# Performance work log

Measured on AMD Instinct MI355X. Metric: run time of the kernel, lower is better.

## Reference

```python
import jax, jax.numpy as jnp
import numpy as np

S = 4096      # seq_len
D = 1024      # d_model
H = 16        # n_heads
E = 64        # head dim (D // H)
SCALE0 = 1.0 / np.sqrt(E)  # sh_scale_factor


def setup_inputs() -> dict:
    key = jax.random.key(0)
    ks = jax.random.split(key, 10)
    std = 1.0 / np.sqrt(D)
    inputs = jax.random.normal(ks[0], (S, D), dtype=jnp.float32)
    # per-head projection weights stacked over heads: [H, D, E]
    Wq = jax.random.normal(ks[1], (H, D, E), dtype=jnp.float32) * std
    bq = jnp.zeros((H, E), dtype=jnp.float32)
    Wk = jax.random.normal(ks[2], (H, D, E), dtype=jnp.float32) * std
    bk = jnp.zeros((H, E), dtype=jnp.float32)
    Wv = jax.random.normal(ks[3], (H, D, E), dtype=jnp.float32) * std
    bv = jnp.zeros((H, E), dtype=jnp.float32)
    # learned per-head scalar scale, initialized to 1/sqrt(E)
    scale = jnp.full((H,), SCALE0, dtype=jnp.float32)
    # output projection (stored as [D_in, D_out])
    Wo = jax.random.normal(ks[4], (H * E, D), dtype=jnp.float32) * std
    bo = jnp.zeros((D,), dtype=jnp.float32)
    return {"inputs": inputs, "Wq": Wq, "bq": bq, "Wk": Wk, "bk": bk,
            "Wv": Wv, "bv": bv, "scale": scale, "Wo": Wo, "bo": bo}


def reference(inputs, Wq, bq, Wk, bk, Wv, bv, scale, Wo, bo):
    # per-head QKV projections, batched over heads: [H, S, E]
    q = jnp.einsum('sd,hde->hse', inputs, Wq) + bq[:, None, :]
    k = jnp.einsum('sd,hde->hse', inputs, Wk) + bk[:, None, :]
    v = jnp.einsum('sd,hde->hse', inputs, Wv) + bv[:, None, :]
    # scores [H, S, S], learned scalar scale per head, softmax over keys
    scores = jnp.einsum('hqe,hke->hqk', q, k) * scale[:, None, None]
    attn = jax.nn.softmax(scores, axis=-1)
    o = jnp.einsum('hqk,hke->hqe', attn, v)           # [H, S, E]
    o = jnp.transpose(o, (1, 0, 2)).reshape(S, H * E)  # concat heads on dim 1
    return o @ Wo + bo                                 # [S, D]
```

## Files before the change

kernel.cpp:

```cpp
#include <hip/hip_runtime.h>
#include <stdint.h>

#define S_LEN 4096
#define D_MOD 1024
#define NH    16
#define EH    64

typedef short bf16x8 __attribute__((ext_vector_type(8)));
typedef float f32x4  __attribute__((ext_vector_type(4)));
typedef float f32x16 __attribute__((ext_vector_type(16)));

__device__ __forceinline__ unsigned short f2b(float x){
    uint32_t u = __float_as_uint(x);
    u = (u + 0x7fffu + ((u >> 16) & 1u)) >> 16;
    return (unsigned short)u;
}

__device__ __forceinline__ uint32_t cvtpk_bf16(float lo, float hi){
    uint32_t r;
    asm volatile("v_cvt_pk_bf16_f32 %0, %1, %2" : "=v"(r) : "v"(lo), "v"(hi));
    return r;
}

__device__ __forceinline__ void gld_lds16(const void* g, void* l){
    __builtin_amdgcn_global_load_lds((const __attribute__((address_space(1))) void*)g,
                                     (__attribute__((address_space(3))) void*)l, 16, 0, 0);
}

#define PSWAP_U(a, b) asm volatile("v_permlane32_swap_b32 %0, %1" : "+v"(a), "+v"(b))

__device__ __forceinline__ float vcopy(float x){
    float y;
    asm volatile("v_mov_b32 %0, %1" : "=v"(y) : "v"(x));
    return y;
}
__device__ __forceinline__ float pswap_add(float x){
    uint32_t a = __float_as_uint(x), b = __float_as_uint(vcopy(x));
    PSWAP_U(a, b);
    return __uint_as_float(a) + __uint_as_float(b);
}

#define WAITV4() asm volatile("s_waitcnt vmcnt(4)" ::: "memory")
#define WAITV0() asm volatile("s_waitcnt vmcnt(0)" ::: "memory")
#define CFENCE() asm volatile("" ::: "memory")


__global__ void k_conv_x(const float* __restrict__ x, unsigned short* __restrict__ xb, int n){
    int i = (blockIdx.x * blockDim.x + threadIdx.x) * 4;
    if (i < n){
        float4 v = *(const float4*)(x + i);
        ushort4 o;
        o.x = f2b(v.x); o.y = f2b(v.y); o.z = f2b(v.z); o.w = f2b(v.w);
        *(ushort4*)(xb + i) = o;
    }
}

__global__ void k_conv_w(const float* __restrict__ Wq, const float* __restrict__ Wk,
                         const float* __restrict__ Wv, unsigned short* __restrict__ wt){
    __shared__ float lt[64][65];
    const int tid = threadIdx.x;
    const int d0 = blockIdx.x * 64;
    const int th = blockIdx.y;
    const int t = th >> 4, h = th & 15;
    const float* W = (t == 0) ? Wq : ((t == 1) ? Wk : Wv);
    #pragma unroll
    for (int i = 0; i < 16; i++){
        int idx = tid + 256 * i;
        int dl = idx >> 6, e = idx & 63;
        lt[dl][e] = W[((size_t)((h << 10) + d0 + dl) << 6) + e];
    }
    __syncthreads();
    #pragma unroll
    for (int i = 0; i < 16; i++){
        int idx = tid + 256 * i;
        int eo = idx >> 6, dlo = idx & 63;
        wt[((size_t)((t << 10) + (h << 6) + eo) << 10) + d0 + dlo] = f2b(lt[dlo][eo]);
    }
}

__global__ void k_conv_wo(const float* __restrict__ Wo, unsigned short* __restrict__ wot){
    __shared__ float lt[64][65];
    const int tid = threadIdx.x;
    const int he0 = blockIdx.x * 64, d0 = blockIdx.y * 64;
    #pragma unroll
    for (int i = 0; i < 16; i++){
        int idx = tid + 256 * i;
        int r = idx >> 6, c = idx & 63;
        lt[r][c] = Wo[((size_t)(he0 + r) << 10) + d0 + c];
    }
    __syncthreads();
    #pragma unroll
    for (int i = 0; i < 16; i++){
        int idx = tid + 256 * i;
        int rr = idx >> 6, cc = idx & 63;
        wot[((size_t)(d0 + rr) << 10) + he0 + cc] = f2b(lt[cc][rr]);
    }
}

__global__ void k_tv(const unsigned short* __restrict__ vr, unsigned short* __restrict__ vt){
    __shared__ unsigned short lt[64][66];
    const int tid = threadIdx.x;
    const int s0 = blockIdx.x * 64, h = blockIdx.y;
    #pragma unroll
    for (int i = 0; i < 4; i++){
        int idx = tid + 256 * i;
        int r = idx >> 4, c4 = idx & 15;
        ushort4 v = *(const ushort4*)(vr + (((size_t)(h << 12) + s0 + r) << 6) + c4 * 4);
        lt[r][c4 * 4 + 0] = v.x; lt[r][c4 * 4 + 1] = v.y;
        lt[r][c4 * 4 + 2] = v.z; lt[r][c4 * 4 + 3] = v.w;
    }
    __syncthreads();
    #pragma unroll
    for (int i = 0; i < 4; i++){
        int idx = tid + 256 * i;
        int e = idx >> 4, j4 = idx & 15;
        ushort4 o;
        o.x = lt[j4 * 4 + 0][e]; o.y = lt[j4 * 4 + 1][e];
        o.z = lt[j4 * 4 + 2][e]; o.w = lt[j4 * 4 + 3][e];
        *(ushort4*)(vt + (size_t)((h << 6) + e) * 4096 + s0 + j4 * 4) = o;
    }
}


template<int MODE, int NI>
__global__ __launch_bounds__(256, 4)
void k_gemm(const unsigned short* __restrict__ A, const unsigned short* __restrict__ B, int K,
            unsigned short* __restrict__ qb, unsigned short* __restrict__ kb,
            unsigned short* __restrict__ vr,
            const float* __restrict__ b0, const float* __restrict__ b1, const float* __restrict__ b2,
            const float* __restrict__ scl,
            float* __restrict__ outp, const float* __restrict__ bo){
    __shared__ uint4 lsA4[1024];
    __shared__ uint4 lsB4[NI * 256];
    char* lsA = (char*)lsA4;
    char* lsB = (char*)lsB4;
    const int tid = threadIdx.x;
    const int lane = tid & 63, w = tid >> 6;
    const int lr = lane & 15, lg = lane >> 4;
    const int wm = w >> 1, wn = w & 1;
    const int m0 = blockIdx.y * 128, n0 = blockIdx.x * (32 * NI);
    const int wbase = tid & ~63;

    f32x4 acc[4][NI] = {};

    for (int k0 = 0; k0 < K; k0 += 64){
        __syncthreads();
        #pragma unroll
        for (int i = 0; i < 4; i++){
            int s = tid + 256 * i;
            int row = s >> 3, c = s & 7;
            int cs = c ^ (row & 7);
            gld_lds16(A + (size_t)(m0 + row) * K + k0 + cs * 8, lsA + (wbase + 256 * i) * 16);
        }
        #pragma unroll
        for (int i = 0; i < NI; i++){
            int s = tid + 256 * i;
            int row = s >> 3, c = s & 7;
            int cs = c ^ (row & 7);
            gld_lds16(B + (size_t)(n0 + row) * K + k0 + cs * 8, lsB + (wbase + 256 * i) * 16);
        }
        __syncthreads();
        #pragma unroll
        for (int kc = 0; kc < 2; kc++){
            bf16x8 af[4], bf[NI];
            #pragma unroll
            for (int mi = 0; mi < 4; mi++){
                int row = wm * 64 + mi * 16 + lr;
                int j = kc * 4 + lg;
                af[mi] = *(const bf16x8*)(lsA + row * 128 + (j ^ (row & 7)) * 16);
            }
            #pragma unroll
            for (int ni = 0; ni < NI; ni++){
                int row = wn * (NI * 16) + ni * 16 + lr;
                int j = kc * 4 + lg;
                bf[ni] = *(const bf16x8*)(lsB + row * 128 + (j ^ (row & 7)) * 16);
            }
            #pragma unroll
            for (int mi = 0; mi < 4; mi++)
                #pragma unroll
                for (int ni = 0; ni < NI; ni++)
                    acc[mi][ni] = __builtin_amdgcn_mfma_f32_16x16x32_bf16(af[mi], bf[ni], acc[mi][ni], 0, 0, 0);
        }
    }

    #pragma unroll
    for (int mi = 0; mi < 4; mi++){
        #pragma unroll
        for (int ni = 0; ni < NI; ni++){
            int gnb = n0 + wn * (NI * 16) + ni * 16;
            if (MODE == 0){
                int t = gnb >> 10, h = (gnb >> 6) & 15;
                int e = (gnb & 63) + lr;
                const float* bp = (t == 0) ? b0 : ((t == 1) ? b1 : b2);
                float badd = bp[(h << 6) + e];
                float qs = (t == 0) ? scl[h] * 1.4426950408889634f : 1.0f;
                unsigned short* tgt = (t == 0) ? qb : ((t == 1) ? kb : vr);
                #pragma unroll
                for (int r = 0; r < 4; r++){
                    int gm = m0 + wm * 64 + mi * 16 + lg * 4 + r;
                    tgt[((size_t)((h << 12) + gm) << 6) + e] = f2b((acc[mi][ni][r] + badd) * qs);
                }
            } else {
                int gn = gnb + lr;
                float badd = bo[gn];
                #pragma unroll
                for (int r = 0; r < 4; r++){
                    int gm = m0 + wm * 64 + mi * 16 + lg * 4 + r;
                    outp[(size_t)gm * 1024 + gn] = acc[mi][ni][r] + badd;
                }
            }
        }
    }
}


__global__ __launch_bounds__(256, 4)
void k_attn(const unsigned short* __restrict__ qb, const unsigned short* __restrict__ kb,
            const unsigned short* __restrict__ vt,
            unsigned short* __restrict__ po0, unsigned short* __restrict__ po1,
            float* __restrict__ pl){
    __shared__ uint4 ldsb[2048];
    char* ldsc = (char*)ldsb;

    const int tid = threadIdx.x;
    const int lane = tid & 63, w = tid >> 6;
    const int ql = lane & 31, hi = lane >> 5;

    int wg = blockIdx.y * 64 + blockIdx.x;
    wg = (wg & 7) * 128 + (wg >> 3);
    const int h = wg >> 6;
    const int qblk = (wg & 63) >> 1;
    const int sk = wg & 1;
    const int q0 = qblk * 128 + w * 32;
    const int kbase = sk * 2048;

    bf16x8 qf[4];
    #pragma unroll
    for (int kc = 0; kc < 4; kc++)
        qf[kc] = *(const bf16x8*)(qb + (size_t)((h << 12) + q0 + ql) * 64 + kc * 16 + hi * 8);

    f32x16 oacc[2] = {};
    float l_run = 0.f;

    auto stage = [&](int buf, int kt){
        char* Kd = ldsc + buf * 16384;
        char* Vd = Kd + 8192;
        #pragma unroll
        for (int c = 0; c < 2; c++){
            int g = w * 2 + c;
            const unsigned short* ksrc = kb + ((size_t)(h << 12) + kt + (g >> 2) * 32 + ql) * 64
                                            + (g & 3) * 16 + hi * 8;
            gld_lds16(ksrc, Kd + g * 1024);
            const unsigned short* vsrc = vt + (size_t)((h << 6) + (g >> 2) * 32 + ql) * 4096
                                            + kt + (g & 3) * 16 + hi * 8;
            gld_lds16(vsrc, Vd + g * 1024);
        }
    };

    stage(0, kbase);
    stage(1, kbase + 64);

    int buf = 0;
    for (int t = 0; t < 32; t++){
        if (t < 31) WAITV4();
        else        WAITV0();
        __builtin_amdgcn_s_barrier();
        CFENCE();

        const char* Kc = ldsc + buf * 16384;
        const char* Vc = Kc + 8192;

        f32x16 s[2];
        __builtin_amdgcn_s_setprio(1);
        #pragma unroll
        for (int kt2 = 0; kt2 < 2; kt2++){
            f32x16 sx = {};
            #pragma unroll
            for (int kc = 0; kc < 4; kc++){
                bf16x8 kf = *(const bf16x8*)(Kc + (kt2 * 4 + kc) * 1024 + lane * 16);
                sx = __builtin_amdgcn_mfma_f32_32x32x16_bf16(kf, qf[kc], sx, 0, 0, 0);
            }
            s[kt2] = sx;
        }
        __builtin_amdgcn_s_setprio(0);

        #pragma unroll
        for (int kt2 = 0; kt2 < 2; kt2++){
            f32x16& v = s[kt2];
            #pragma unroll
            for (int r = 0; r < 16; r++){
                v[r] = __builtin_amdgcn_exp2f(v[r]);
                l_run += v[r];
            }
            uint32_t a0 = cvtpk_bf16(v[0], v[1]);
            uint32_t a1 = cvtpk_bf16(v[2], v[3]);
            uint32_t b0 = cvtpk_bf16(v[4], v[5]);
            uint32_t b1 = cvtpk_bf16(v[6], v[7]);
            PSWAP_U(a0, b0);
            PSWAP_U(a1, b1);
            uint32_t f0[4] = {a0, a1, b0, b1};
            bf16x8 p0 = *(bf16x8*)f0;
            uint32_t c0 = cvtpk_bf16(v[8],  v[9]);
            uint32_t c1 = cvtpk_bf16(v[10], v[11]);
            uint32_t d0 = cvtpk_bf16(v[12], v[13]);
            uint32_t d1 = cvtpk_bf16(v[14], v[15]);
            PSWAP_U(c0, d0);
            PSWAP_U(c1, d1);
            uint32_t f1[4] = {c0, c1, d0, d1};
            bf16x8 p1 = *(bf16x8*)f1;

            #pragma unroll
            for (int et = 0; et < 2; et++){
                bf16x8 vf0 = *(const bf16x8*)(Vc + (et * 4 + kt2 * 2) * 1024 + lane * 16);
                oacc[et] = __builtin_amdgcn_mfma_f32_32x32x16_bf16(vf0, p0, oacc[et], 0, 0, 0);
                bf16x8 vf1 = *(const bf16x8*)(Vc + (et * 4 + kt2 * 2 + 1) * 1024 + lane * 16);
                oacc[et] = __builtin_amdgcn_mfma_f32_32x32x16_bf16(vf1, p1, oacc[et], 0, 0, 0);
            }
        }
        CFENCE();

        if (t + 2 < 32){
            __builtin_amdgcn_s_barrier();
            CFENCE();
            stage(buf, kbase + (t + 2) * 64);
        }
        buf ^= 1;
    }

    unsigned short* pout = sk ? po1 : po0;
    float l = pswap_add(l_run);
    if (lane < 32)
        pl[((sk << 4) + h) * 4096 + q0 + ql] = l;
    #pragma unroll
    for (int et = 0; et < 2; et++){
        #pragma unroll
        for (int g = 0; g < 4; g++){
            ushort4 o4;
            o4.x = f2b(oacc[et][4 * g + 0]);
            o4.y = f2b(oacc[et][4 * g + 1]);
            o4.z = f2b(oacc[et][4 * g + 2]);
            o4.w = f2b(oacc[et][4 * g + 3]);
            int e = et * 32 + 8 * g + 4 * hi;
            *(ushort4*)(pout + (size_t)(q0 + ql) * 1024 + (h << 6) + e) = o4;
        }
    }
}

__global__ void k_comb(const unsigned short* __restrict__ po0, const unsigned short* __restrict__ po1,
                       const float* __restrict__ pl, unsigned short* __restrict__ ob){
    int i = blockIdx.x * 256 + threadIdx.x;
    int s = i >> 7, g8 = i & 127;
    int h = g8 >> 3;
    float inv = 1.0f / (pl[(h << 12) + s] + pl[((16 + h) << 12) + s]);
    size_t off = ((size_t)s << 10) + g8 * 8;
    const ushort4* a = (const ushort4*)(po0 + off);
    const ushort4* b = (const ushort4*)(po1 + off);
    ushort4 o[2];
    #pragma unroll
    for (int k = 0; k < 2; k++){
        ushort4 av = a[k], bv = b[k];
        o[k].x = f2b((__uint_as_float((uint32_t)av.x << 16) + __uint_as_float((uint32_t)bv.x << 16)) * inv);
        o[k].y = f2b((__uint_as_float((uint32_t)av.y << 16) + __uint_as_float((uint32_t)bv.y << 16)) * inv);
        o[k].z = f2b((__uint_as_float((uint32_t)av.z << 16) + __uint_as_float((uint32_t)bv.z << 16)) * inv);
        o[k].w = f2b((__uint_as_float((uint32_t)av.w << 16) + __uint_as_float((uint32_t)bv.w << 16)) * inv);
    }
    *(ushort4*)(ob + off) = o[0];
    *(ushort4*)(ob + off + 4) = o[1];
}


extern "C" void kernel_launch(void* const* d_in, const int* in_sizes, int n_in,
                              void* d_out, int out_size, void* d_ws, size_t ws_size,
                              hipStream_t stream){
    const float* x  = (const float*)d_in[0];
    const float* Wq = (const float*)d_in[1];
    const float* bq = (const float*)d_in[2];
    const float* Wk = (const float*)d_in[3];
    const float* bk = (const float*)d_in[4];
    const float* Wv = (const float*)d_in[5];
    const float* bv = (const float*)d_in[6];
    const float* sc = (const float*)d_in[7];
    const float* Wo = (const float*)d_in[8];
    const float* bo = (const float*)d_in[9];
    float* out = (float*)d_out;
    char* ws = (char*)d_ws;
    const size_t MB = 1u << 20;

    unsigned short* xb  = (unsigned short*)(ws + 0);
    unsigned short* ob  = xb;
    unsigned short* wt  = (unsigned short*)(ws + 8  * MB);
    unsigned short* wot = (unsigned short*)(ws + 14 * MB);
    unsigned short* qb  = (unsigned short*)(ws + 16 * MB);
    unsigned short* kb  = (unsigned short*)(ws + 24 * MB);
    unsigned short* vr  = (unsigned short*)(ws + 32 * MB);
    unsigned short* po0 = vr;
    unsigned short* vt  = (unsigned short*)(ws + 40 * MB);
    unsigned short* po1 = (unsigned short*)(ws + 48 * MB);
    float*          pl  = (float*)(ws + 56 * MB);

    k_conv_x <<<4096, 256, 0, stream>>>(x, xb, S_LEN * D_MOD);
    k_conv_w <<<dim3(16, 48), 256, 0, stream>>>(Wq, Wk, Wv, wt);
    k_conv_wo<<<dim3(16, 16), 256, 0, stream>>>(Wo, wot);

    k_gemm<0, 4><<<dim3(24, 32), 256, 0, stream>>>(xb, wt, D_MOD, qb, kb, vr, bq, bk, bv, sc, nullptr, nullptr);
    k_tv        <<<dim3(64, 16), 256, 0, stream>>>(vr, vt);
    k_attn      <<<dim3(64, 16), 256, 0, stream>>>(qb, kb, vt, po0, po1, pl);
    k_comb      <<<2048, 256, 0, stream>>>(po0, po1, pl, ob);
    k_gemm<1, 2><<<dim3(16, 32), 256, 0, stream>>>(ob, wot, D_MOD, nullptr, nullptr, nullptr,
                                                   nullptr, nullptr, nullptr, nullptr, out, bo);
}
```

Baseline: 162.8 us.

## Merge conversion kernels and compute softmax row sums via ones-MFMA

Three conversion kernels (x, QKV weights, Wo) become one launch that picks its role from the block index, removing two launch gaps. In attention, the running softmax denominator is no longer a per-element VALU sum plus a final cross-lane reduce. It is accumulated by extra MFMAs against a vector of bf16 ones, which offloads VALU work to the matrix unit. The QK and PV stages are also interleaved per 32-key half so the exp/pack of one half can overlap matrix work. This adds 4 MFMAs per tile and sums bf16-rounded probabilities instead of fp32 values, a small accuracy change.

```diff
diff --git a/kernel.cpp b/kernel.cpp
--- a/kernel.cpp
+++ b/kernel.cpp
@@ -29,71 +29,61 @@
 
 #define PSWAP_U(a, b) asm volatile("v_permlane32_swap_b32 %0, %1" : "+v"(a), "+v"(b))
 
-__device__ __forceinline__ float vcopy(float x){
-    float y;
-    asm volatile("v_mov_b32 %0, %1" : "=v"(y) : "v"(x));
-    return y;
-}
-__device__ __forceinline__ float pswap_add(float x){
-    uint32_t a = __float_as_uint(x), b = __float_as_uint(vcopy(x));
-    PSWAP_U(a, b);
-    return __uint_as_float(a) + __uint_as_float(b);
-}
-
 #define WAITV4() asm volatile("s_waitcnt vmcnt(4)" ::: "memory")
 #define WAITV0() asm volatile("s_waitcnt vmcnt(0)" ::: "memory")
 #define CFENCE() asm volatile("" ::: "memory")
 
 
-__global__ void k_conv_x(const float* __restrict__ x, unsigned short* __restrict__ xb, int n){
-    int i = (blockIdx.x * blockDim.x + threadIdx.x) * 4;
-    if (i < n){
+__global__ void k_conv_all(const float* __restrict__ x, unsigned short* __restrict__ xb,
+                           const float* __restrict__ Wq, const float* __restrict__ Wk,
+                           const float* __restrict__ Wv, unsigned short* __restrict__ wt,
+                           const float* __restrict__ Wo, unsigned short* __restrict__ wot){
+    __shared__ float lt[64][65];
+    const int tid = threadIdx.x;
+    int b = blockIdx.x;
+    if (b < 4096){
+        int i = (b * 256 + tid) * 4;
         float4 v = *(const float4*)(x + i);
         ushort4 o;
         o.x = f2b(v.x); o.y = f2b(v.y); o.z = f2b(v.z); o.w = f2b(v.w);
         *(ushort4*)(xb + i) = o;
-    }
-}
-
-__global__ void k_conv_w(const float* __restrict__ Wq, const float* __restrict__ Wk,
-                         const float* __restrict__ Wv, unsigned short* __restrict__ wt){
-    __shared__ float lt[64][65];
-    const int tid = threadIdx.x;
-    const int d0 = blockIdx.x * 64;
-    const int th = blockIdx.y;
-    const int t = th >> 4, h = th & 15;
-    const float* W = (t == 0) ? Wq : ((t == 1) ? Wk : Wv);
-    #pragma unroll
-    for (int i = 0; i < 16; i++){
-        int idx = tid + 256 * i;
-        int dl = idx >> 6, e = idx & 63;
-        lt[dl][e] = W[((size_t)((h << 10) + d0 + dl) << 6) + e];
-    }
-    __syncthreads();
-    #pragma unroll
-    for (int i = 0; i < 16; i++){
-        int idx = tid + 256 * i;
-        int eo = idx >> 6, dlo = idx & 63;
-        wt[((size_t)((t << 10) + (h << 6) + eo) << 10) + d0 + dlo] = f2b(lt[dlo][eo]);
-    }
-}
-
-__global__ void k_conv_wo(const float* __restrict__ Wo, unsigned short* __restrict__ wot){
-    __shared__ float lt[64][65];
-    const int tid = threadIdx.x;
-    const int he0 = blockIdx.x * 64, d0 = blockIdx.y * 64;
-    #pragma unroll
-    for (int i = 0; i < 16; i++){
-        int idx = tid + 256 * i;
-        int r = idx >> 6, c = idx & 63;
-        lt[r][c] = Wo[((size_t)(he0 + r) << 10) + d0 + c];
-    }
-    __syncthreads();
-    #pragma unroll
-    for (int i = 0; i < 16; i++){
-        int idx = tid + 256 * i;
-        int rr = idx >> 6, cc = idx & 63;
-        wot[((size_t)(d0 + rr) << 10) + he0 + cc] = f2b(lt[cc][rr]);
+        return;
+    }
+    b -= 4096;
+    if (b < 768){
+        const int d0 = (b & 15) * 64;
+        const int th = b >> 4;
+        const int t = th >> 4, h = th & 15;
+        const float* W = (t == 0) ? Wq : ((t == 1) ? Wk : Wv);
+        #pragma unroll
+        for (int i = 0; i < 16; i++){
+            int idx = tid + 256 * i;
+            int dl = idx >> 6, e = idx & 63;
+            lt[dl][e] = W[((size_t)((h << 10) + d0 + dl) << 6) + e];
+        }
+        __syncthreads();
+        #pragma unroll
+        for (int i = 0; i < 16; i++){
+            int idx = tid + 256 * i;
+            int eo = idx >> 6, dlo = idx & 63;
+            wt[((size_t)((t << 10) + (h << 6) + eo) << 10) + d0 + dlo] = f2b(lt[dlo][eo]);
+        }
+    } else {
+        b -= 768;
+        const int he0 = (b & 15) * 64, d0 = (b >> 4) * 64;
+        #pragma unroll
+        for (int i = 0; i < 16; i++){
+            int idx = tid + 256 * i;
+            int r = idx >> 6, c = idx & 63;
+            lt[r][c] = Wo[((size_t)(he0 + r) << 10) + d0 + c];
+        }
+        __syncthreads();
+        #pragma unroll
+        for (int i = 0; i < 16; i++){
+            int idx = tid + 256 * i;
+            int rr = idx >> 6, cc = idx & 63;
+            wot[((size_t)(d0 + rr) << 10) + he0 + cc] = f2b(lt[cc][rr]);
+        }
     }
 }
 
@@ -239,8 +229,11 @@
     for (int kc = 0; kc < 4; kc++)
         qf[kc] = *(const bf16x8*)(qb + (size_t)((h << 12) + q0 + ql) * 64 + kc * 16 + hi * 8);
 
-    f32x16 oacc[2] = {};
-    float l_run = 0.f;
+    bf16x8 ones;
+    #pragma unroll
+    for (int j = 0; j < 8; j++) ones[j] = (short)0x3F80;
+
+    f32x16 oacc[2] = {}, lacc = {};
 
     auto stage = [&](int buf, int kt){
         char* Kd = ldsc + buf * 16384;
@@ -257,6 +250,28 @@
         }
     };
 
+    auto pack2 = [&](f32x16& v, bf16x8& pA, bf16x8& pB){
+        #pragma unroll
+        for (int r = 0; r < 16; r++)
+            v[r] = __builtin_amdgcn_exp2f(v[r]);
+        uint32_t a0 = cvtpk_bf16(v[0], v[1]);
+        uint32_t a1 = cvtpk_bf16(v[2], v[3]);
+        uint32_t b0 = cvtpk_bf16(v[4], v[5]);
+        uint32_t b1 = cvtpk_bf16(v[6], v[7]);
+        PSWAP_U(a0, b0);
+        PSWAP_U(a1, b1);
+        uint32_t f0[4] = {a0, a1, b0, b1};
+        pA = *(bf16x8*)f0;
+        uint32_t c0 = cvtpk_bf16(v[8],  v[9]);
+        uint32_t c1 = cvtpk_bf16(v[10], v[11]);
+        uint32_t d0 = cvtpk_bf16(v[12], v[13]);
+        uint32_t d1 = cvtpk_bf16(v[14], v[15]);
+        PSWAP_U(c0, d0);
+        PSWAP_U(c1, d1);
+        uint32_t f1[4] = {c0, c1, d0, d1};
+        pB = *(bf16x8*)f1;
+    };
+
     stage(0, kbase);
     stage(1, kbase + 64);
 
@@ -270,53 +285,49 @@
         const char* Kc = ldsc + buf * 16384;
         const char* Vc = Kc + 8192;
 
-        f32x16 s[2];
+        f32x16 s0 = {}, s1 = {};
         __builtin_amdgcn_s_setprio(1);
         #pragma unroll
-        for (int kt2 = 0; kt2 < 2; kt2++){
-            f32x16 sx = {};
-            #pragma unroll
-            for (int kc = 0; kc < 4; kc++){
-                bf16x8 kf = *(const bf16x8*)(Kc + (kt2 * 4 + kc) * 1024 + lane * 16);
-                sx = __builtin_amdgcn_mfma_f32_32x32x16_bf16(kf, qf[kc], sx, 0, 0, 0);
-            }
-            s[kt2] = sx;
+        for (int kc = 0; kc < 4; kc++){
+            bf16x8 kf = *(const bf16x8*)(Kc + kc * 1024 + lane * 16);
+            s0 = __builtin_amdgcn_mfma_f32_32x32x16_bf16(kf, qf[kc], s0, 0, 0, 0);
+        }
+        #pragma unroll
+        for (int kc = 0; kc < 4; kc++){
+            bf16x8 kf = *(const bf16x8*)(Kc + (4 + kc) * 1024 + lane * 16);
+            s1 = __builtin_amdgcn_mfma_f32_32x32x16_bf16(kf, qf[kc], s1, 0, 0, 0);
+        }
+        bf16x8 p00, p01;
+        pack2(s0, p00, p01);
+
+        {
+            bf16x8 vf0 = *(const bf16x8*)(Vc + (0 * 4 + 0) * 1024 + lane * 16);
+            oacc[0] = __builtin_amdgcn_mfma_f32_32x32x16_bf16(vf0, p00, oacc[0], 0, 0, 0);
+            bf16x8 vf1 = *(const bf16x8*)(Vc + (1 * 4 + 0) * 1024 + lane * 16);
+            oacc[1] = __builtin_amdgcn_mfma_f32_32x32x16_bf16(vf1, p00, oacc[1], 0, 0, 0);
+            lacc = __builtin_amdgcn_mfma_f32_32x32x16_bf16(ones, p00, lacc, 0, 0, 0);
+            bf16x8 vf2 = *(const bf16x8*)(Vc + (0 * 4 + 1) * 1024 + lane * 16);
+            oacc[0] = __builtin_amdgcn_mfma_f32_32x32x16_bf16(vf2, p01, oacc[0], 0, 0, 0);
+            bf16x8 vf3 = *(const bf16x8*)(Vc + (1 * 4 + 1) * 1024 + lane * 16);
+            oacc[1] = __builtin_amdgcn_mfma_f32_32x32x16_bf16(vf3, p01, oacc[1], 0, 0, 0);
+            lacc = __builtin_amdgcn_mfma_f32_32x32x16_bf16(ones, p01, lacc, 0, 0, 0);
+        }
+        bf16x8 p10, p11;
+        pack2(s1, p10, p11);
+
+        {
+            bf16x8 vf0 = *(const bf16x8*)(Vc + (0 * 4 + 2) * 1024 + lane * 16);
+            oacc[0] = __builtin_amdgcn_mfma_f32_32x32x16_bf16(vf0, p10, oacc[0], 0, 0, 0);
+            bf16x8 vf1 = *(const bf16x8*)(Vc + (1 * 4 + 2) * 1024 + lane * 16);
+            oacc[1] = __builtin_amdgcn_mfma_f32_32x32x16_bf16(vf1, p10, oacc[1], 0, 0, 0);
+            lacc = __builtin_amdgcn_mfma_f32_32x32x16_bf16(ones, p10, lacc, 0, 0, 0);
+            bf16x8 vf2 = *(const bf16x8*)(Vc + (0 * 4 + 3) * 1024 + lane * 16);
+            oacc[0] = __builtin_amdgcn_mfma_f32_32x32x16_bf16(vf2, p11, oacc[0], 0, 0, 0);
+            bf16x8 vf3 = *(const bf16x8*)(Vc + (1 * 4 + 3) * 1024 + lane * 16);
+            oacc[1] = __builtin_amdgcn_mfma_f32_32x32x16_bf16(vf3, p11, oacc[1], 0, 0, 0);
+            lacc = __builtin_amdgcn_mfma_f32_32x32x16_bf16(ones, p11, lacc, 0, 0, 0);
         }
         __builtin_amdgcn_s_setprio(0);
-
-        #pragma unroll
-        for (int kt2 = 0; kt2 < 2; kt2++){
-            f32x16& v = s[kt2];
-            #pragma unroll
-            for (int r = 0; r < 16; r++){
-                v[r] = __builtin_amdgcn_exp2f(v[r]);
-                l_run += v[r];
-            }
-            uint32_t a0 = cvtpk_bf16(v[0], v[1]);
-            uint32_t a1 = cvtpk_bf16(v[2], v[3]);
-            uint32_t b0 = cvtpk_bf16(v[4], v[5]);
-            uint32_t b1 = cvtpk_bf16(v[6], v[7]);
-            PSWAP_U(a0, b0);
-            PSWAP_U(a1, b1);
-            uint32_t f0[4] = {a0, a1, b0, b1};
-            bf16x8 p0 = *(bf16x8*)f0;
-            uint32_t c0 = cvtpk_bf16(v[8],  v[9]);
-            uint32_t c1 = cvtpk_bf16(v[10], v[11]);
-            uint32_t d0 = cvtpk_bf16(v[12], v[13]);
-            uint32_t d1 = cvtpk_bf16(v[14], v[15]);
-            PSWAP_U(c0, d0);
-            PSWAP_U(c1, d1);
-            uint32_t f1[4] = {c0, c1, d0, d1};
-            bf16x8 p1 = *(bf16x8*)f1;
-
-            #pragma unroll
-            for (int et = 0; et < 2; et++){
-                bf16x8 vf0 = *(const bf16x8*)(Vc + (et * 4 + kt2 * 2) * 1024 + lane * 16);
-                oacc[et] = __builtin_amdgcn_mfma_f32_32x32x16_bf16(vf0, p0, oacc[et], 0, 0, 0);
-                bf16x8 vf1 = *(const bf16x8*)(Vc + (et * 4 + kt2 * 2 + 1) * 1024 + lane * 16);
-                oacc[et] = __builtin_amdgcn_mfma_f32_32x32x16_bf16(vf1, p1, oacc[et], 0, 0, 0);
-            }
-        }
         CFENCE();
 
         if (t + 2 < 32){
@@ -328,9 +339,8 @@
     }
 
     unsigned short* pout = sk ? po1 : po0;
-    float l = pswap_add(l_run);
     if (lane < 32)
-        pl[((sk << 4) + h) * 4096 + q0 + ql] = l;
+        pl[((sk << 4) + h) * 4096 + q0 + ql] = lacc[0];
     #pragma unroll
     for (int et = 0; et < 2; et++){
         #pragma unroll
@@ -398,9 +408,7 @@
     unsigned short* po1 = (unsigned short*)(ws + 48 * MB);
     float*          pl  = (float*)(ws + 56 * MB);
 
-    k_conv_x <<<4096, 256, 0, stream>>>(x, xb, S_LEN * D_MOD);
-    k_conv_w <<<dim3(16, 48), 256, 0, stream>>>(Wq, Wk, Wv, wt);
-    k_conv_wo<<<dim3(16, 16), 256, 0, stream>>>(Wo, wot);
+    k_conv_all<<<5120, 256, 0, stream>>>(x, xb, Wq, Wk, Wv, wt, Wo, wot);
 
     k_gemm<0, 4><<<dim3(24, 32), 256, 0, stream>>>(xb, wt, D_MOD, qb, kb, vr, bq, bk, bv, sc, nullptr, nullptr);
     k_tv        <<<dim3(64, 16), 256, 0, stream>>>(vr, vt);
```

Measured after the change: 160.0 us. No clear change (-1.7%).
